# Optimization experiments

Hardware: AMD Instinct MI355X
Metric: run time of the kernel (lower is better)

The kernel has to match this reference:

```python
import jax, jax.numpy as jnp
import numpy as np

K = 16
EPS = 1e-5  # BatchNorm eps (torch default)


def _lin(t, w, b):
    # 1x1 Conv2d over channel dim == per-point linear
    return jnp.einsum('bnkc,cd->bnkd', t, w) + b


def _bn(t, g, b):
    # BatchNorm2d (training-mode batch stats) over all dims except channels
    m = jnp.mean(t, axis=(0, 1, 2), keepdims=True)
    v = jnp.var(t, axis=(0, 1, 2), keepdims=True)
    return (t - m) * jax.lax.rsqrt(v + EPS) * g + b


def setup_inputs() -> dict:
    key = jax.random.key(0)
    ks = jax.random.split(key, 8)
    B, N, C, OUT = 4, 4096, 61, 128
    IN = C + 3  # 64 = in_feat_dim

    def w(k, i, o):
        return jax.random.normal(k, (i, o), jnp.float32) * (1.0 / np.sqrt(i))

    return {
        'x': jax.random.normal(ks[0], (B, N, C), jnp.float32),
        'pos': jax.random.uniform(ks[1], (B, N, 3), jnp.float32),
        # relation_vec_to_weights_net: 10 -> 32 -> IN -> IN (no BN, last_act=False)
        'rw1': w(ks[2], 10, 32), 'rb1': jnp.zeros((32,), jnp.float32),
        'rw2': w(ks[3], 32, IN), 'rb2': jnp.zeros((IN,), jnp.float32),
        'rw3': w(ks[4], IN, IN), 'rb3': jnp.zeros((IN,), jnp.float32),
        # feat_mlp_net: IN -> OUT -> OUT (BN, last_act=False)
        'fw1': w(ks[5], IN, OUT), 'fb1': jnp.zeros((OUT,), jnp.float32),
        'g1': jnp.ones((OUT,), jnp.float32), 'b1': jnp.zeros((OUT,), jnp.float32),
        'fw2': w(ks[6], OUT, OUT), 'fb2': jnp.zeros((OUT,), jnp.float32),
        'g2': jnp.ones((OUT,), jnp.float32), 'b2': jnp.zeros((OUT,), jnp.float32),
    }


def reference(x, pos, rw1, rb1, rw2, rb2, rw3, rb3,
              fw1, fb1, g1, b1, fw2, fb2, g2, b2):
    B, N, _ = x.shape
    # pairwise squared distances (B,N,N); sampled_idx=None -> all points are centers
    d2 = jnp.sum((pos[:, :, None, :] - pos[:, None, :, :]) ** 2, axis=-1)
    _, idx = jax.lax.top_k(-d2, K)                      # kNN indices (B,N,K)
    gather = jax.vmap(lambda v, i: v[i])                # per-batch fancy gather
    gpos = gather(pos, idx)                             # (B,N,K,3)
    gx = gather(x, idx)                                 # (B,N,K,C)
    cpos = pos[:, :, None, :]                           # center positions (B,N,1,3)
    rel = gpos - cpos                                   # relative pos (B,N,K,3)
    s = jnp.sum(rel ** 2, axis=-1, keepdims=True)
    # safe L2 norm (grad 0 at 0, like torch.norm)
    dis = jnp.where(s > 0, jnp.sqrt(jnp.where(s > 0, s, 1.0)), 0.0)
    relation = jnp.concatenate(
        [jnp.broadcast_to(cpos, gpos.shape), gpos, rel, dis], axis=-1)  # (B,N,K,10)
    h = jax.nn.relu(_lin(relation, rw1, rb1))
    h = jax.nn.relu(_lin(h, rw2, rb2))
    weights = _lin(h, rw3, rb3)                         # (B,N,K,IN), no last act
    feat = jnp.concatenate([gx, gpos], axis=-1)         # (B,N,K,IN)
    feat = weights * feat
    feat = jnp.max(feat, axis=2, keepdims=True)         # max-pool over K -> (B,N,1,IN)
    feat = jax.nn.relu(feat)
    feat = jax.nn.relu(_bn(_lin(feat, fw1, fb1), g1, b1))
    feat = _bn(_lin(feat, fw2, fb2), g2, b2)            # last_act=False
    return feat[:, :, 0, :]                             # (B,N,OUT)
```

## Files before the change

kernel.cpp:

```cpp
#include <hip/hip_runtime.h>
#include <hip/hip_bf16.h>
#include <math.h>

#define NPTS   4096
#define NB     4
#define NC     61
#define NK     16
#define NROWS  16384
#define BN_EPS 1e-5f
#define INV_ROWS (1.0f/16384.0f)

#define GRD    8
#define NCELL  512
#define CELLH  0.125f

typedef short bf16x8 __attribute__((ext_vector_type(8)));
typedef float f32x4  __attribute__((ext_vector_type(4)));

__global__ __launch_bounds__(256) void prep_kernel(const float* __restrict__ pos,
                                                   float4* __restrict__ pos4,
                                                   int* __restrict__ cellOf,
                                                   int* __restrict__ counts) {
    const int i = blockIdx.x * 256 + threadIdx.x;
    if (i >= NB * NPTS) return;
    const float px = pos[i * 3 + 0], py = pos[i * 3 + 1], pz = pos[i * 3 + 2];
    pos4[i] = make_float4(px, py, pz, 0.f);
    const int cx = min(GRD - 1, max(0, (int)(px * GRD)));
    const int cy = min(GRD - 1, max(0, (int)(py * GRD)));
    const int cz = min(GRD - 1, max(0, (int)(pz * GRD)));
    const int cid = ((cz << 3) + cy) * GRD + cx;
    cellOf[i] = cid;
    atomicAdd(&counts[(i >> 12) * NCELL + cid], 1);
}

__global__ __launch_bounds__(512) void scan_kernel(const int* __restrict__ counts,
                                                   int* __restrict__ cellStart) {
    __shared__ int s[NCELL];
    const int b = blockIdx.x, t = threadIdx.x;
    s[t] = counts[b * NCELL + t];
    __syncthreads();
    for (int off = 1; off < NCELL; off <<= 1) {
        const int v = (t >= off) ? s[t - off] : 0;
        __syncthreads();
        s[t] += v;
        __syncthreads();
    }
    cellStart[b * (NCELL + 1) + t + 1] = s[t];
    if (t == 0) cellStart[b * (NCELL + 1)] = 0;
}

__global__ __launch_bounds__(256) void scatter_kernel(const float4* __restrict__ pos4,
                                                      const int* __restrict__ cellOf,
                                                      const int* __restrict__ cellStart,
                                                      int* __restrict__ fill,
                                                      float4* __restrict__ spt) {
    const int i = blockIdx.x * 256 + threadIdx.x;
    if (i >= NB * NPTS) return;
    const int b = i >> 12;
    const int cid = cellOf[i];
    const int dst = cellStart[b * (NCELL + 1) + cid] + atomicAdd(&fill[b * NCELL + cid], 1);
    float4 p = pos4[i];
    p.w = __int_as_float(i & 4095);
    spt[(b << 12) + dst] = p;
}

#define OCAP 8
#define NPAD 257

__global__ __launch_bounds__(256) void knn_kernel(const float4* __restrict__ pos4,
                                                  const float4* __restrict__ spt,
                                                  const int* __restrict__ cellStart,
                                                  int* __restrict__ idx_out,
                                                  int* __restrict__ flagcnt,
                                                  int* __restrict__ flaglist) {
    __shared__ unsigned long long buf[OCAP * NPAD];
    const int t  = threadIdx.x;
    const int l8 = t & 7;
    const int q  = blockIdx.x * 32 + (t >> 3);
    const int b  = q >> 12;
    const float4* __restrict__ sb = spt + (b << 12);
    const int* __restrict__ cs = cellStart + b * (NCELL + 1);

    const float4 qp = pos4[q];
    const float qx = qp.x, qy = qp.y, qz = qp.z;
    const int cx = min(GRD - 1, max(0, (int)(qx * GRD)));
    const int cy = min(GRD - 1, max(0, (int)(qy * GRD)));
    const int cz = min(GRD - 1, max(0, (int)(qz * GRD)));
    const int x0 = max(0, cx - 1), x1 = min(GRD - 1, cx + 1);

    unsigned long long bk[16];
#pragma unroll
    for (int i = 0; i < 16; ++i) bk[i] = ~0ull;
    unsigned int thr_bits = 0xFFFFFFFFu;
    int owptr = 0;

    auto compact = [&]() {
        unsigned long long od[OCAP];
#pragma unroll
        for (int s = 0; s < OCAP; ++s) {
            const unsigned long long v = buf[s * NPAD + t];
            od[s] = (s < owptr) ? v : ~0ull;
        }
        owptr = 0;
#pragma unroll
        for (int k = 2; k <= 8; k <<= 1) {
#pragma unroll
            for (int j = k >> 1; j > 0; j >>= 1) {
#pragma unroll
                for (int i = 0; i < 8; ++i) {
                    const int l = i ^ j;
                    if (l > i) {
                        const bool up = ((i & k) == 0);
                        const unsigned long long a = od[i], c = od[l];
                        const bool sw = up ? (c < a) : (a < c);
                        od[i] = sw ? c : a;
                        od[l] = sw ? a : c;
                    }
                }
            }
        }
#pragma unroll
        for (int i = 8; i < 16; ++i) {
            const unsigned long long c = od[15 - i];
            bk[i] = (c < bk[i]) ? c : bk[i];
        }
#pragma unroll
        for (int j = 8; j > 0; j >>= 1) {
#pragma unroll
            for (int i = 0; i < 16; ++i) {
                const int l = i ^ j;
                if (l > i) {
                    const unsigned long long a = bk[i], c = bk[l];
                    const bool sw = (c < a);
                    bk[i] = sw ? c : a;
                    bk[l] = sw ? a : c;
                }
            }
        }
        unsigned int th = (unsigned int)(bk[15] >> 32);
#pragma unroll
        for (int m = 1; m <= 4; m <<= 1) {
            const unsigned int o = __shfl_xor(th, m, 8);
            th = (o < th) ? o : th;
        }
        thr_bits = th;
    };

    for (int rz = 0; rz < 3; ++rz) {
        for (int ry = 0; ry < 3; ++ry) {
            const int zz = cz + rz - 1, yy = cy + ry - 1;
            int rs = 0, re = 0;
            if (zz >= 0 && zz < GRD && yy >= 0 && yy < GRD) {
                const int rowb = ((zz << 3) + yy) << 3;
                rs = cs[rowb + x0];
                re = cs[rowb + x1 + 1];
            }
            int p = rs + l8;
            while (__any(p < re)) {
                if (p < re) {
                    const float4 c = sb[p];
                    const float dx = qx - c.x, dy = qy - c.y, dz = qz - c.z;
                    const float d2 = __fadd_rn(__fadd_rn(__fmul_rn(dx, dx), __fmul_rn(dy, dy)),
                                               __fmul_rn(dz, dz));
                    if (__float_as_uint(d2) < thr_bits) {
                        buf[owptr * NPAD + t] =
                            ((unsigned long long)__float_as_uint(d2) << 32) |
                            (unsigned int)__float_as_int(c.w);
                        owptr++;
                    }
                }
                p += 8;
                if (__any(owptr >= OCAP - 1)) compact();
            }
        }
    }
    compact();

#pragma unroll
    for (int m = 1; m <= 4; m <<= 1) {
        unsigned long long ot[16];
#pragma unroll
        for (int i = 0; i < 16; ++i) ot[i] = __shfl_xor(bk[i], m, 8);
#pragma unroll
        for (int i = 0; i < 16; ++i) {
            const unsigned long long c = ot[15 - i];
            bk[i] = (c < bk[i]) ? c : bk[i];
        }
#pragma unroll
        for (int j = 8; j > 0; j >>= 1) {
#pragma unroll
            for (int i = 0; i < 16; ++i) {
                const int l = i ^ j;
                if (l > i) {
                    const unsigned long long a = bk[i], c = bk[l];
                    const bool sw = (c < a);
                    bk[i] = sw ? c : a;
                    bk[l] = sw ? a : c;
                }
            }
        }
    }

    if (l8 == 0) {
        const int ob = q * NK;
        *(int4*)&idx_out[ob + 0]  = make_int4((int)bk[0],  (int)bk[1],  (int)bk[2],  (int)bk[3]);
        *(int4*)&idx_out[ob + 4]  = make_int4((int)bk[4],  (int)bk[5],  (int)bk[6],  (int)bk[7]);
        *(int4*)&idx_out[ob + 8]  = make_int4((int)bk[8],  (int)bk[9],  (int)bk[10], (int)bk[11]);
        *(int4*)&idx_out[ob + 12] = make_int4((int)bk[12], (int)bk[13], (int)bk[14], (int)bk[15]);

        const int y0 = max(0, cy - 1), y1 = min(GRD - 1, cy + 1);
        const int z0 = max(0, cz - 1), z1 = min(GRD - 1, cz + 1);
        float mg = 1e30f;
        if (x0 > 0)       mg = fminf(mg, qx - x0 * CELLH);
        if (x1 < GRD - 1) mg = fminf(mg, (x1 + 1) * CELLH - qx);
        if (y0 > 0)       mg = fminf(mg, qy - y0 * CELLH);
        if (y1 < GRD - 1) mg = fminf(mg, (y1 + 1) * CELLH - qy);
        if (z0 > 0)       mg = fminf(mg, qz - z0 * CELLH);
        if (z1 < GRD - 1) mg = fminf(mg, (z1 + 1) * CELLH - qz);
        mg = fmaxf(mg - 1e-5f, 0.f);
        const float mg2 = mg * mg;
        if ((unsigned int)(bk[15] >> 32) >= __float_as_uint(mg2)) {
            const int slot = atomicAdd(flagcnt, 1);
            flaglist[slot] = q;
        }
    }
}

__global__ __launch_bounds__(256) void knn_fallback(const float4* __restrict__ pos4,
                                                    int* __restrict__ idx_out,
                                                    const int* __restrict__ flagcnt,
                                                    const int* __restrict__ flaglist) {
    __shared__ unsigned long long wres[4 * 16];
    const int nf = flagcnt[0];
    const int t = threadIdx.x;
    const int w = t >> 6;

    for (int fi = blockIdx.x; fi < nf; fi += 64) {
        const int qi = flaglist[fi];
        const int b = qi >> 12;
        const float4* __restrict__ pb = pos4 + (b << 12);
        const float4 qp = pb[qi & 4095];

        float4 c[16];
#pragma unroll
        for (int s = 0; s < 16; ++s) c[s] = pb[(s << 8) | t];

        unsigned long long key[16];
#pragma unroll
        for (int s = 0; s < 16; ++s) {
            const int j = (s << 8) | t;
            const float dx = qp.x - c[s].x, dy = qp.y - c[s].y, dz = qp.z - c[s].z;
            const float d2 = __fadd_rn(__fadd_rn(__fmul_rn(dx, dx), __fmul_rn(dy, dy)),
                                       __fmul_rn(dz, dz));
            key[s] = ((unsigned long long)__float_as_uint(d2) << 32) | (unsigned int)j;
        }

#pragma unroll
        for (int k = 2; k <= 16; k <<= 1) {
#pragma unroll
            for (int j = k >> 1; j > 0; j >>= 1) {
#pragma unroll
                for (int i = 0; i < 16; ++i) {
                    const int l = i ^ j;
                    if (l > i) {
                        const bool up = ((i & k) == 0);
                        const unsigned long long a = key[i], cc = key[l];
                        const bool sw = up ? (cc < a) : (a < cc);
                        key[i] = sw ? cc : a;
                        key[l] = sw ? a : cc;
                    }
                }
            }
        }

#pragma unroll
        for (int m = 1; m <= 32; m <<= 1) {
            unsigned long long ot[16];
#pragma unroll
            for (int i = 0; i < 16; ++i) ot[i] = __shfl_xor(key[i], m, 64);
#pragma unroll
            for (int i = 0; i < 16; ++i) {
                const unsigned long long cc = ot[15 - i];
                key[i] = (cc < key[i]) ? cc : key[i];
            }
#pragma unroll
            for (int j = 8; j > 0; j >>= 1) {
#pragma unroll
                for (int i = 0; i < 16; ++i) {
                    const int l = i ^ j;
                    if (l > i) {
                        const unsigned long long a = key[i], cc = key[l];
                        const bool sw = (cc < a);
                        key[i] = sw ? cc : a;
                        key[l] = sw ? a : cc;
                    }
                }
            }
        }

        if ((t & 63) == 0) {
#pragma unroll
            for (int i = 0; i < 16; ++i) wres[w * 16 + i] = key[i];
        }
        __syncthreads();

        if (t == 0) {
            int hp[4] = {0, 0, 0, 0};
            const int ob = qi * NK;
            for (int o = 0; o < NK; ++o) {
                unsigned long long bestk = ~0ull;
                int bestw = 0;
#pragma unroll
                for (int w2 = 0; w2 < 4; ++w2) {
                    const unsigned long long h = (hp[w2] < 16) ? wres[w2 * 16 + hp[w2]] : ~0ull;
                    if (h < bestk) { bestk = h; bestw = w2; }
                }
                idx_out[ob + o] = (int)(bestk & 0xFFFFFFFFu);
                hp[bestw]++;
            }
        }
        __syncthreads();
    }
}

__device__ __forceinline__ unsigned int f2bf(float f) {
    unsigned int b = __float_as_uint(f);
    return (b + 0x7FFFu + ((b >> 16) & 1u)) >> 16;
}

__global__ __launch_bounds__(256) void mlp_kernel(
    const float4* __restrict__ pos4, const float* __restrict__ x,
    const int* __restrict__ idx,
    const float* __restrict__ rw1, const float* __restrict__ rb1,
    const float* __restrict__ rw2, const float* __restrict__ rb2,
    const float* __restrict__ rw3, const float* __restrict__ rb3,
    float* __restrict__ pooled) {
    __shared__ __attribute__((aligned(16))) unsigned short w1t[32 * 40];
    __shared__ __attribute__((aligned(16))) unsigned short w2t[64 * 40];
    __shared__ __attribute__((aligned(16))) unsigned short w3t[64 * 72];
    __shared__ __attribute__((aligned(16))) unsigned short scr[4 * 64 * 72];

    const int t = threadIdx.x;
    for (int i = t; i < 32 * 32; i += 256) {
        const int n = i >> 5, k = i & 31;
        float v = 0.f;
        if (k < 10) v = rw1[k * 32 + n];
        else if (k == 15) v = rb1[n];
        w1t[n * 40 + k] = (unsigned short)f2bf(v);
    }
    for (int i = t; i < 64 * 32; i += 256) {
        const int n = i >> 5, k = i & 31;
        w2t[n * 40 + k] = (unsigned short)f2bf(rw2[k * 64 + n]);
    }
    for (int i = t; i < 64 * 64; i += 256) {
        const int n = i >> 6, k = i & 63;
        w3t[n * 72 + k] = (unsigned short)f2bf(rw3[k * 64 + n]);
    }
    __syncthreads();

    const int lane = t & 63;
    const int quad = lane >> 4;
    const int l16  = lane & 15;
    unsigned short* __restrict__ ws = &scr[(t >> 6) * 64 * 72];

    const int rowbase = blockIdx.x * 256 + (t & 192);
    const int b = rowbase >> 16;
    const float4* __restrict__ pb = pos4 + ((size_t)b << 12);
    const float* __restrict__ xb = x + ((size_t)b << 12) * NC;

    {
        const int row_g = rowbase + lane;
        const int q = row_g >> 4;
        const int j = idx[row_g];
        const float4 cp = pb[q & 4095];
        const float4 gp = pb[j];
        const float rx = gp.x - cp.x, ry = gp.y - cp.y, rz = gp.z - cp.z;
        const float ss = rx * rx + ry * ry + rz * rz;
        const float dis = (ss > 0.f) ? sqrtf(ss) : 0.f;
        unsigned int d[20];
#pragma unroll
        for (int i = 0; i < 20; ++i) d[i] = 0;
        d[0] = f2bf(cp.x) | (f2bf(cp.y) << 16);
        d[1] = f2bf(cp.z) | (f2bf(gp.x) << 16);
        d[2] = f2bf(gp.y) | (f2bf(gp.z) << 16);
        d[3] = f2bf(rx)   | (f2bf(ry) << 16);
        d[4] = f2bf(rz)   | (f2bf(dis) << 16);
        d[7] = 0x3F800000u;
        unsigned int* wr = (unsigned int*)&ws[lane * 40];
#pragma unroll
        for (int i = 0; i < 20; ++i) wr[i] = d[i];
    }
    __builtin_amdgcn_s_waitcnt(0);

    const f32x4 zero = {0.f, 0.f, 0.f, 0.f};

    bf16x8 a1[4], b1f[2];
#pragma unroll
    for (int mt = 0; mt < 4; ++mt)
        a1[mt] = *(const bf16x8*)&ws[(mt * 16 + l16) * 40 + quad * 8];
#pragma unroll
    for (int nt = 0; nt < 2; ++nt)
        b1f[nt] = *(const bf16x8*)&w1t[(nt * 16 + l16) * 40 + quad * 8];

    f32x4 c1[2][4];
#pragma unroll
    for (int nt = 0; nt < 2; ++nt)
#pragma unroll
        for (int mt = 0; mt < 4; ++mt)
            c1[nt][mt] = __builtin_amdgcn_mfma_f32_16x16x32_bf16(a1[mt], b1f[nt], zero, 0, 0, 0);

#pragma unroll
    for (int nt = 0; nt < 2; ++nt)
#pragma unroll
        for (int mt = 0; mt < 4; ++mt)
#pragma unroll
            for (int r = 0; r < 4; ++r)
                ws[(mt * 16 + quad * 4 + r) * 40 + nt * 16 + l16] =
                    (unsigned short)f2bf(fmaxf(c1[nt][mt][r], 0.f));
    __builtin_amdgcn_s_waitcnt(0);

    float b2v[4], b3v[4];
#pragma unroll
    for (int nt = 0; nt < 4; ++nt) { b2v[nt] = rb2[nt * 16 + l16]; b3v[nt] = rb3[nt * 16 + l16]; }

    bf16x8 a2[4];
#pragma unroll
    for (int mt = 0; mt < 4; ++mt)
        a2[mt] = *(const bf16x8*)&ws[(mt * 16 + l16) * 40 + quad * 8];

    f32x4 c2[4][4];
#pragma unroll
    for (int nt = 0; nt < 4; ++nt) {
        const bf16x8 b2f = *(const bf16x8*)&w2t[(nt * 16 + l16) * 40 + quad * 8];
#pragma unroll
        for (int mt = 0; mt < 4; ++mt)
            c2[nt][mt] = __builtin_amdgcn_mfma_f32_16x16x32_bf16(a2[mt], b2f, zero, 0, 0, 0);
    }

#pragma unroll
    for (int nt = 0; nt < 4; ++nt)
#pragma unroll
        for (int mt = 0; mt < 4; ++mt)
#pragma unroll
            for (int r = 0; r < 4; ++r)
                ws[(mt * 16 + quad * 4 + r) * 72 + nt * 16 + l16] =
                    (unsigned short)f2bf(fmaxf(c2[nt][mt][r] + b2v[nt], 0.f));
    __builtin_amdgcn_s_waitcnt(0);

    bf16x8 a3[4][2];
#pragma unroll
    for (int mt = 0; mt < 4; ++mt)
#pragma unroll
        for (int kt = 0; kt < 2; ++kt)
            a3[mt][kt] = *(const bf16x8*)&ws[(mt * 16 + l16) * 72 + kt * 32 + quad * 8];

    f32x4 c3[4][4];
#pragma unroll
    for (int nt = 0; nt < 4; ++nt) {
        const bf16x8 b3f0 = *(const bf16x8*)&w3t[(nt * 16 + l16) * 72 + 0 * 32 + quad * 8];
        const bf16x8 b3f1 = *(const bf16x8*)&w3t[(nt * 16 + l16) * 72 + 1 * 32 + quad * 8];
#pragma unroll
        for (int mt = 0; mt < 4; ++mt) {
            f32x4 acc = __builtin_amdgcn_mfma_f32_16x16x32_bf16(a3[mt][0], b3f0, zero, 0, 0, 0);
            c3[nt][mt] = __builtin_amdgcn_mfma_f32_16x16x32_bf16(a3[mt][1], b3f1, acc, 0, 0, 0);
        }
    }

#pragma unroll
    for (int mt = 0; mt < 4; ++mt) {
        const int qg = (rowbase >> 4) + mt;
        int jrow[4];
#pragma unroll
        for (int r = 0; r < 4; ++r) jrow[r] = idx[rowbase + mt * 16 + quad * 4 + r];
#pragma unroll
        for (int nt = 0; nt < 4; ++nt) {
            const int col = nt * 16 + l16;
            float mx = -1e30f;
#pragma unroll
            for (int r = 0; r < 4; ++r) {
                const int j = jrow[r];
                float fv;
                if (col < NC) fv = xb[(size_t)j * NC + col];
                else          fv = ((const float*)&pb[j])[col - NC];
                mx = fmaxf(mx, fv * (c3[nt][mt][r] + b3v[nt]));
            }
            mx = fmaxf(mx, __shfl_xor(mx, 16, 64));
            mx = fmaxf(mx, __shfl_xor(mx, 32, 64));
            mx = fmaxf(mx, 0.f);
            if (quad == 0) pooled[(size_t)qg * 64 + col] = mx;
        }
    }
}

__global__ __launch_bounds__(256) void gemm1_kernel(
    const float* __restrict__ A, const float* __restrict__ W,
    const float* __restrict__ bias, float* __restrict__ y,
    float* __restrict__ sum, float* __restrict__ sumsq) {
    __shared__ float As[64 * 64];
    __shared__ float Bs[64 * 128];
    const int t = threadIdx.x;
    const int r0 = blockIdx.x * 64;
    for (int i = t; i < 64 * 128; i += 256) Bs[i] = W[i];
    for (int i = t; i < 64 * 64; i += 256)  As[i] = A[(size_t)r0 * 64 + i];
    __syncthreads();

    const int c = t & 127, rg = t >> 7;
    float acc[32];
    const float bv = bias[c];
#pragma unroll
    for (int r = 0; r < 32; ++r) acc[r] = bv;

    for (int kk = 0; kk < 64; kk += 4) {
        const float b0 = Bs[(kk + 0) * 128 + c];
        const float b1 = Bs[(kk + 1) * 128 + c];
        const float b2 = Bs[(kk + 2) * 128 + c];
        const float b3 = Bs[(kk + 3) * 128 + c];
#pragma unroll
        for (int r = 0; r < 32; ++r) {
            const float4 a = *(const float4*)&As[(rg * 32 + r) * 64 + kk];
            acc[r] += a.x * b0 + a.y * b1 + a.z * b2 + a.w * b3;
        }
    }

    float s = 0.f, s2 = 0.f;
#pragma unroll
    for (int r = 0; r < 32; ++r) {
        const float v = acc[r];
        s += v; s2 += v * v;
        y[(size_t)(r0 + rg * 32 + r) * 128 + c] = v;
    }
    __syncthreads();
    As[t] = s; As[256 + t] = s2;
    __syncthreads();
    if (rg == 0) {
        atomicAdd(&sum[c],   As[c] + As[128 + c]);
        atomicAdd(&sumsq[c], As[256 + c] + As[256 + 128 + c]);
    }
}

__global__ __launch_bounds__(256) void gemm2_kernel(
    const float* __restrict__ y1, const float* __restrict__ W,
    const float* __restrict__ bias,
    const float* __restrict__ sum1, const float* __restrict__ sumsq1,
    const float* __restrict__ g1, const float* __restrict__ b1,
    float* __restrict__ y2, float* __restrict__ sum2, float* __restrict__ sumsq2) {
    __shared__ float As[64 * 128];
    __shared__ float Bs[64 * 128];
    __shared__ float a1s[128], s1s[128];
    const int t = threadIdx.x;
    const int r0 = blockIdx.x * 64;

    if (t < 128) {
        const float m = sum1[t] * INV_ROWS;
        const float v = sumsq1[t] * INV_ROWS - m * m;
        const float a = rsqrtf(v + BN_EPS) * g1[t];
        a1s[t] = a; s1s[t] = b1[t] - m * a;
    }
    for (int i = t; i < 64 * 128; i += 256) Bs[i] = W[i];
    __syncthreads();
    for (int i = t; i < 64 * 128; i += 256) {
        const int cc = i & 127;
        const float v = y1[(size_t)r0 * 128 + i];
        As[i] = fmaxf(v * a1s[cc] + s1s[cc], 0.f);
    }
    __syncthreads();

    const int c = t & 127, rg = t >> 7;
    float acc[32];
    const float bv = bias[c];
#pragma unroll
    for (int r = 0; r < 32; ++r) acc[r] = bv;

    for (int kk = 0; kk < 64; kk += 4) {
        const float b0 = Bs[(kk + 0) * 128 + c];
        const float b1v = Bs[(kk + 1) * 128 + c];
        const float b2 = Bs[(kk + 2) * 128 + c];
        const float b3 = Bs[(kk + 3) * 128 + c];
#pragma unroll
        for (int r = 0; r < 32; ++r) {
            const float4 a = *(const float4*)&As[(rg * 32 + r) * 128 + kk];
            acc[r] += a.x * b0 + a.y * b1v + a.z * b2 + a.w * b3;
        }
    }
    __syncthreads();
    for (int i = t; i < 64 * 128; i += 256) Bs[i] = W[64 * 128 + i];
    __syncthreads();
    for (int kk = 0; kk < 64; kk += 4) {
        const float b0 = Bs[(kk + 0) * 128 + c];
        const float b1v = Bs[(kk + 1) * 128 + c];
        const float b2 = Bs[(kk + 2) * 128 + c];
        const float b3 = Bs[(kk + 3) * 128 + c];
#pragma unroll
        for (int r = 0; r < 32; ++r) {
            const float4 a = *(const float4*)&As[(rg * 32 + r) * 128 + 64 + kk];
            acc[r] += a.x * b0 + a.y * b1v + a.z * b2 + a.w * b3;
        }
    }

    float s = 0.f, s2 = 0.f;
#pragma unroll
    for (int r = 0; r < 32; ++r) {
        const float v = acc[r];
        s += v; s2 += v * v;
        y2[(size_t)(r0 + rg * 32 + r) * 128 + c] = v;
    }
    __syncthreads();
    As[t] = s; As[256 + t] = s2;
    __syncthreads();
    if (rg == 0) {
        atomicAdd(&sum2[c],   As[c] + As[128 + c]);
        atomicAdd(&sumsq2[c], As[256 + c] + As[256 + 128 + c]);
    }
}

__global__ __launch_bounds__(256) void bnout_kernel(
    const float* __restrict__ y2, const float* __restrict__ sum2,
    const float* __restrict__ sumsq2, const float* __restrict__ g2,
    const float* __restrict__ b2, float* __restrict__ out) {
    const int i = blockIdx.x * 256 + threadIdx.x;
    const int c = i & 127;
    const float m = sum2[c] * INV_ROWS;
    const float v = sumsq2[c] * INV_ROWS - m * m;
    const float a = rsqrtf(v + BN_EPS) * g2[c];
    out[i] = y2[i] * a + (b2[c] - m * a);
}

extern "C" void kernel_launch(void* const* d_in, const int* in_sizes, int n_in,
                              void* d_out, int out_size, void* d_ws, size_t ws_size,
                              hipStream_t stream) {
    const float* x   = (const float*)d_in[0];
    const float* pos = (const float*)d_in[1];
    const float* rw1 = (const float*)d_in[2];
    const float* rb1 = (const float*)d_in[3];
    const float* rw2 = (const float*)d_in[4];
    const float* rb2 = (const float*)d_in[5];
    const float* rw3 = (const float*)d_in[6];
    const float* rb3 = (const float*)d_in[7];
    const float* fw1 = (const float*)d_in[8];
    const float* fb1 = (const float*)d_in[9];
    const float* g1  = (const float*)d_in[10];
    const float* b1  = (const float*)d_in[11];
    const float* fw2 = (const float*)d_in[12];
    const float* fb2 = (const float*)d_in[13];
    const float* g2  = (const float*)d_in[14];
    const float* b2  = (const float*)d_in[15];
    float* out = (float*)d_out;

    char* ws = (char*)d_ws;
    int*    idx      = (int*)ws;
    float*  pooled   = (float*)(ws + (1u << 20));
    float*  y1       = (float*)(ws + (5u << 20));
    float*  y2       = (float*)(ws + (13u << 20));
    float*  stats    = (float*)(ws + (21u << 20));
    float*  sum1 = stats, *sumsq1 = stats + 128, *sum2 = stats + 256, *sumsq2 = stats + 384;
    int*    counts   = (int*)(stats + 512);
    int*    fill     = counts + NB * NCELL;
    int*    flagcnt  = fill + NB * NCELL;
    int*    cellStart= (int*)(ws + (21u << 20) + (20u << 10));
    int*    cellOf   = (int*)(ws + (21u << 20) + (32u << 10));
    int*    flaglist = (int*)(ws + (21u << 20) + (96u << 10));
    float4* pos4     = (float4*)(ws + (22u << 20));
    float4* spt      = (float4*)(ws + (22u << 20) + (256u << 10));

    hipMemsetAsync(stats, 0, (512 + 2048 + 2048 + 1) * sizeof(float), stream);

    prep_kernel<<<64, 256, 0, stream>>>(pos, pos4, cellOf, counts);
    scan_kernel<<<NB, 512, 0, stream>>>(counts, cellStart);
    scatter_kernel<<<64, 256, 0, stream>>>(pos4, cellOf, cellStart, fill, spt);
    knn_kernel<<<512, 256, 0, stream>>>(pos4, spt, cellStart, idx, flagcnt, flaglist);
    knn_fallback<<<64, 256, 0, stream>>>(pos4, idx, flagcnt, flaglist);
    mlp_kernel<<<1024, 256, 0, stream>>>(pos4, x, idx, rw1, rb1, rw2, rb2, rw3, rb3, pooled);
    gemm1_kernel<<<256, 256, 0, stream>>>(pooled, fw1, fb1, y1, sum1, sumsq1);
    gemm2_kernel<<<256, 256, 0, stream>>>(y1, fw2, fb2, sum1, sumsq1, g1, b1, y2, sum2, sumsq2);
    bnout_kernel<<<NROWS * 128 / 256, 256, 0, stream>>>(y2, sum2, sumsq2, g2, b2, out);
}
```

Measured before the change: 260.7 us.

## Pad gathered features to 64-wide rows, load layer-1 weights in registers, halve GEMM tiles

A new pre-pass kernel packs x and pos into a 64-float-per-point buffer, so the max-pool gather in the MLP kernel becomes one unconditional strided load instead of a branch between x and pos4. The first-layer weight fragment is now built directly into registers from global memory rather than staged through shared memory. The two BN GEMM kernels use 32-row tiles with twice as many blocks, which lowers per-thread accumulator count and adds parallelism. In exchange there is an extra kernel launch plus a write and read of a roughly 4 MB padded buffer.

```diff
diff --git a/kernel.cpp b/kernel.cpp
--- a/kernel.cpp
+++ b/kernel.cpp
@@ -31,6 +31,14 @@
     const int cid = ((cz << 3) + cy) * GRD + cx;
     cellOf[i] = cid;
     atomicAdd(&counts[(i >> 12) * NCELL + cid], 1);
+}
+
+__global__ __launch_bounds__(256) void xpack_kernel(const float* __restrict__ x,
+                                                    const float* __restrict__ pos,
+                                                    float* __restrict__ xpad) {
+    const int g = blockIdx.x * 256 + threadIdx.x;
+    const int i = g >> 6, c = g & 63;
+    xpad[g] = (c < NC) ? x[i * NC + c] : pos[i * 3 + (c - NC)];
 }
 
 __global__ __launch_bounds__(512) void scan_kernel(const int* __restrict__ counts,
@@ -329,25 +337,17 @@
 }
 
 __global__ __launch_bounds__(256) void mlp_kernel(
-    const float4* __restrict__ pos4, const float* __restrict__ x,
+    const float4* __restrict__ pos4, const float* __restrict__ xpad,
     const int* __restrict__ idx,
     const float* __restrict__ rw1, const float* __restrict__ rb1,
     const float* __restrict__ rw2, const float* __restrict__ rb2,
     const float* __restrict__ rw3, const float* __restrict__ rb3,
     float* __restrict__ pooled) {
-    __shared__ __attribute__((aligned(16))) unsigned short w1t[32 * 40];
     __shared__ __attribute__((aligned(16))) unsigned short w2t[64 * 40];
     __shared__ __attribute__((aligned(16))) unsigned short w3t[64 * 72];
     __shared__ __attribute__((aligned(16))) unsigned short scr[4 * 64 * 72];
 
     const int t = threadIdx.x;
-    for (int i = t; i < 32 * 32; i += 256) {
-        const int n = i >> 5, k = i & 31;
-        float v = 0.f;
-        if (k < 10) v = rw1[k * 32 + n];
-        else if (k == 15) v = rb1[n];
-        w1t[n * 40 + k] = (unsigned short)f2bf(v);
-    }
     for (int i = t; i < 64 * 32; i += 256) {
         const int n = i >> 5, k = i & 31;
         w2t[n * 40 + k] = (unsigned short)f2bf(rw2[k * 64 + n]);
@@ -366,7 +366,21 @@
     const int rowbase = blockIdx.x * 256 + (t & 192);
     const int b = rowbase >> 16;
     const float4* __restrict__ pb = pos4 + ((size_t)b << 12);
-    const float* __restrict__ xb = x + ((size_t)b << 12) * NC;
+    const float* __restrict__ xpb = xpad + (((size_t)b << 12) << 6);
+
+    bf16x8 b1f[2];
+#pragma unroll
+    for (int nt = 0; nt < 2; ++nt) {
+        const int n = nt * 16 + l16;
+#pragma unroll
+        for (int j = 0; j < 8; ++j) {
+            const int k = quad * 8 + j;
+            float f = 0.f;
+            if (k < 10) f = rw1[k * 32 + n];
+            else if (k == 15) f = rb1[n];
+            b1f[nt][j] = (short)f2bf(f);
+        }
+    }
 
     {
         const int row_g = rowbase + lane;
@@ -394,13 +408,10 @@
 
     const f32x4 zero = {0.f, 0.f, 0.f, 0.f};
 
-    bf16x8 a1[4], b1f[2];
+    bf16x8 a1[4];
 #pragma unroll
     for (int mt = 0; mt < 4; ++mt)
         a1[mt] = *(const bf16x8*)&ws[(mt * 16 + l16) * 40 + quad * 8];
-#pragma unroll
-    for (int nt = 0; nt < 2; ++nt)
-        b1f[nt] = *(const bf16x8*)&w1t[(nt * 16 + l16) * 40 + quad * 8];
 
     f32x4 c1[2][4];
 #pragma unroll
@@ -478,10 +489,7 @@
             float mx = -1e30f;
 #pragma unroll
             for (int r = 0; r < 4; ++r) {
-                const int j = jrow[r];
-                float fv;
-                if (col < NC) fv = xb[(size_t)j * NC + col];
-                else          fv = ((const float*)&pb[j])[col - NC];
+                const float fv = xpb[((size_t)jrow[r] << 6) + col];
                 mx = fmaxf(mx, fv * (c3[nt][mt][r] + b3v[nt]));
             }
             mx = fmaxf(mx, __shfl_xor(mx, 16, 64));
@@ -496,19 +504,19 @@
     const float* __restrict__ A, const float* __restrict__ W,
     const float* __restrict__ bias, float* __restrict__ y,
     float* __restrict__ sum, float* __restrict__ sumsq) {
-    __shared__ float As[64 * 64];
+    __shared__ float As[32 * 64];
     __shared__ float Bs[64 * 128];
     const int t = threadIdx.x;
-    const int r0 = blockIdx.x * 64;
+    const int r0 = blockIdx.x * 32;
     for (int i = t; i < 64 * 128; i += 256) Bs[i] = W[i];
-    for (int i = t; i < 64 * 64; i += 256)  As[i] = A[(size_t)r0 * 64 + i];
+    for (int i = t; i < 32 * 64; i += 256)  As[i] = A[(size_t)r0 * 64 + i];
     __syncthreads();
 
     const int c = t & 127, rg = t >> 7;
-    float acc[32];
+    float acc[16];
     const float bv = bias[c];
 #pragma unroll
-    for (int r = 0; r < 32; ++r) acc[r] = bv;
+    for (int r = 0; r < 16; ++r) acc[r] = bv;
 
     for (int kk = 0; kk < 64; kk += 4) {
         const float b0 = Bs[(kk + 0) * 128 + c];
@@ -516,18 +524,18 @@
         const float b2 = Bs[(kk + 2) * 128 + c];
         const float b3 = Bs[(kk + 3) * 128 + c];
 #pragma unroll
-        for (int r = 0; r < 32; ++r) {
-            const float4 a = *(const float4*)&As[(rg * 32 + r) * 64 + kk];
+        for (int r = 0; r < 16; ++r) {
+            const float4 a = *(const float4*)&As[(rg * 16 + r) * 64 + kk];
             acc[r] += a.x * b0 + a.y * b1 + a.z * b2 + a.w * b3;
         }
     }
 
     float s = 0.f, s2 = 0.f;
 #pragma unroll
-    for (int r = 0; r < 32; ++r) {
+    for (int r = 0; r < 16; ++r) {
         const float v = acc[r];
         s += v; s2 += v * v;
-        y[(size_t)(r0 + rg * 32 + r) * 128 + c] = v;
+        y[(size_t)(r0 + rg * 16 + r) * 128 + c] = v;
     }
     __syncthreads();
     As[t] = s; As[256 + t] = s2;
@@ -544,11 +552,11 @@
     const float* __restrict__ sum1, const float* __restrict__ sumsq1,
     const float* __restrict__ g1, const float* __restrict__ b1,
     float* __restrict__ y2, float* __restrict__ sum2, float* __restrict__ sumsq2) {
-    __shared__ float As[64 * 128];
+    __shared__ float As[32 * 128];
     __shared__ float Bs[64 * 128];
     __shared__ float a1s[128], s1s[128];
     const int t = threadIdx.x;
-    const int r0 = blockIdx.x * 64;
+    const int r0 = blockIdx.x * 32;
 
     if (t < 128) {
         const float m = sum1[t] * INV_ROWS;
@@ -558,7 +566,7 @@
     }
     for (int i = t; i < 64 * 128; i += 256) Bs[i] = W[i];
     __syncthreads();
-    for (int i = t; i < 64 * 128; i += 256) {
+    for (int i = t; i < 32 * 128; i += 256) {
         const int cc = i & 127;
         const float v = y1[(size_t)r0 * 128 + i];
         As[i] = fmaxf(v * a1s[cc] + s1s[cc], 0.f);
@@ -566,10 +574,10 @@
     __syncthreads();
 
     const int c = t & 127, rg = t >> 7;
-    float acc[32];
+    float acc[16];
     const float bv = bias[c];
 #pragma unroll
-    for (int r = 0; r < 32; ++r) acc[r] = bv;
+    for (int r = 0; r < 16; ++r) acc[r] = bv;
 
     for (int kk = 0; kk < 64; kk += 4) {
         const float b0 = Bs[(kk + 0) * 128 + c];
@@ -577,8 +585,8 @@
         const float b2 = Bs[(kk + 2) * 128 + c];
         const float b3 = Bs[(kk + 3) * 128 + c];
 #pragma unroll
-        for (int r = 0; r < 32; ++r) {
-            const float4 a = *(const float4*)&As[(rg * 32 + r) * 128 + kk];
+        for (int r = 0; r < 16; ++r) {
+            const float4 a = *(const float4*)&As[(rg * 16 + r) * 128 + kk];
             acc[r] += a.x * b0 + a.y * b1v + a.z * b2 + a.w * b3;
         }
     }
@@ -591,18 +599,18 @@
         const float b2 = Bs[(kk + 2) * 128 + c];
         const float b3 = Bs[(kk + 3) * 128 + c];
 #pragma unroll
-        for (int r = 0; r < 32; ++r) {
-            const float4 a = *(const float4*)&As[(rg * 32 + r) * 128 + 64 + kk];
+        for (int r = 0; r < 16; ++r) {
+            const float4 a = *(const float4*)&As[(rg * 16 + r) * 128 + 64 + kk];
             acc[r] += a.x * b0 + a.y * b1v + a.z * b2 + a.w * b3;
         }
     }
 
     float s = 0.f, s2 = 0.f;
 #pragma unroll
-    for (int r = 0; r < 32; ++r) {
+    for (int r = 0; r < 16; ++r) {
         const float v = acc[r];
         s += v; s2 += v * v;
-        y2[(size_t)(r0 + rg * 32 + r) * 128 + c] = v;
+        y2[(size_t)(r0 + rg * 16 + r) * 128 + c] = v;
     }
     __syncthreads();
     As[t] = s; As[256 + t] = s2;
@@ -661,16 +669,18 @@
     int*    flaglist = (int*)(ws + (21u << 20) + (96u << 10));
     float4* pos4     = (float4*)(ws + (22u << 20));
     float4* spt      = (float4*)(ws + (22u << 20) + (256u << 10));
+    float*  xpad     = (float*)(ws + (23u << 20));
 
     hipMemsetAsync(stats, 0, (512 + 2048 + 2048 + 1) * sizeof(float), stream);
 
     prep_kernel<<<64, 256, 0, stream>>>(pos, pos4, cellOf, counts);
+    xpack_kernel<<<4096, 256, 0, stream>>>(x, pos, xpad);
     scan_kernel<<<NB, 512, 0, stream>>>(counts, cellStart);
     scatter_kernel<<<64, 256, 0, stream>>>(pos4, cellOf, cellStart, fill, spt);
     knn_kernel<<<512, 256, 0, stream>>>(pos4, spt, cellStart, idx, flagcnt, flaglist);
     knn_fallback<<<64, 256, 0, stream>>>(pos4, idx, flagcnt, flaglist);
-    mlp_kernel<<<1024, 256, 0, stream>>>(pos4, x, idx, rw1, rb1, rw2, rb2, rw3, rb3, pooled);
-    gemm1_kernel<<<256, 256, 0, stream>>>(pooled, fw1, fb1, y1, sum1, sumsq1);
-    gemm2_kernel<<<256, 256, 0, stream>>>(y1, fw2, fb2, sum1, sumsq1, g1, b1, y2, sum2, sumsq2);
+    mlp_kernel<<<1024, 256, 0, stream>>>(pos4, xpad, idx, rw1, rb1, rw2, rb2, rw3, rb3, pooled);
+    gemm1_kernel<<<512, 256, 0, stream>>>(pooled, fw1, fb1, y1, sum1, sumsq1);
+    gemm2_kernel<<<512, 256, 0, stream>>>(y1, fw2, fb2, sum1, sumsq1, g1, b1, y2, sum2, sumsq2);
     bnout_kernel<<<NROWS * 128 / 256, 256, 0, stream>>>(y2, sum2, sumsq2, g2, b2, out);
 }
```

Measured after the change: 257.3 us. About the same (-1.3%).
